# Kernel tuning notes

Hardware: AMD Instinct MI355X
Metric: run time of the kernel (lower is better)

Reference implementation:

```python
import jax, jax.numpy as jnp
import numpy as np

B, S, D, F, TOPK = 8, 2048, 1024, 64, 8


def setup_inputs() -> dict:
    key = jax.random.key(0)
    ks = jax.random.split(key, 4)
    scale = 1.0 / np.sqrt(D)
    return {
        "x": jax.random.normal(ks[0], (B, S, D), dtype=jnp.float32),
        "W_top": jax.random.normal(ks[1], (D, F), dtype=jnp.float32) * scale,
        "b_top": jnp.zeros((F,), dtype=jnp.float32),
        "W_feat": jax.random.normal(ks[2], (D, F), dtype=jnp.float32) * scale,
        "b_feat": jnp.zeros((F,), dtype=jnp.float32),
        "W_gates": jax.random.normal(ks[3], (F, D), dtype=jnp.float32) * scale,
        "b_gates": jnp.zeros((F,), dtype=jnp.float32),
        "alpha": jnp.ones((1,), dtype=jnp.float32),
        "num": TOPK,
    }


def reference(x, W_top, b_top, W_feat, b_feat, W_gates, b_gates, alpha, num):
    # Router logits and top-k selection: [B,S,F] -> vals/idx [B,S,num]
    top_logits = jnp.einsum("bsd,df->bsf", x, W_top) + b_top
    vals, idx = jax.lax.top_k(top_logits, num)
    sm = jax.nn.softmax(vals, axis=-1)                     # softmax over selected experts
    # Scatter softmax'd top-k weights into dense [B,S,F] (zeros elsewhere)
    onehot = jax.nn.one_hot(idx, F, dtype=sm.dtype)        # [B,S,num,F]
    type_dense = jnp.einsum("bsk,bskf->bsf", sm, onehot)
    # Dense softmax routing branch
    feat_soft = jax.nn.softmax(jnp.einsum("bsd,df->bsf", x, W_feat) + b_feat, axis=-1)
    a = jax.nn.sigmoid(alpha)                              # [1], broadcasts
    features = a * type_dense + (1.0 - a) * feat_soft      # [B,S,F]
    # num_feature small Linear(dims,1)+Sigmoid gates fused into one GEMM
    gates = jax.nn.sigmoid(jnp.einsum("bsd,fd->bsf", x, W_gates) + b_gates)  # [B,S,F]
    # Weighted sum over feature axis; original returns shape [B,S,1]
    return jnp.sum(gates * features, axis=-1, keepdims=True)
```

## Files before the change

kernel.cpp:

```cpp
#include <hip/hip_runtime.h>
#include <math.h>

#define D_DIM 1024
#define TOKB  32
#define NCH   32

typedef short  bf16x8 __attribute__((ext_vector_type(8)));
typedef float  f32x4  __attribute__((ext_vector_type(4)));

__device__ __forceinline__ ushort f2bf(float f) {
  uint u = __float_as_uint(f);
  return (ushort)((u + 0x7fffu + ((u >> 16) & 1u)) >> 16);
}
__device__ __forceinline__ float bf2f(ushort h) {
  return __uint_as_float(((uint)h) << 16);
}
__device__ __forceinline__ float sigm(float v) {
  return 1.f / (1.f + expf(-v));
}

__global__ __launch_bounds__(256) void pack_w_kernel(
    const float* __restrict__ Wt, const float* __restrict__ Wf,
    const float* __restrict__ Wg, ushort* __restrict__ Wp) {
  int gid = blockIdx.x * 256 + threadIdx.x;
  if (gid >= 32 * 12 * 64 * 4) return;
  int jp   = gid & 3;
  int t    = gid >> 2;
  int lane = t & 63;
  int t2   = t >> 6;
  int fb   = t2 % 12;
  int ks   = t2 / 12;
  int k0   = ks * 32 + ((lane >> 4) << 3) + jp * 2;
  int f    = fb * 16 + (lane & 15);
  float v0, v1;
  if (f < 64)       { v0 = Wt[k0 * 64 + f];            v1 = Wt[(k0 + 1) * 64 + f]; }
  else if (f < 128) { v0 = Wf[k0 * 64 + f - 64];       v1 = Wf[(k0 + 1) * 64 + f - 64]; }
  else              { v0 = Wg[(f - 128) * D_DIM + k0]; v1 = Wg[(f - 128) * D_DIM + k0 + 1]; }
  ushort h0 = f2bf(v0), h1 = f2bf(v1);
  ushort l0 = f2bf(v0 - bf2f(h0)), l1 = f2bf(v1 - bf2f(h1));
  size_t base = ((size_t)(ks * 12 + fb) * 2) * 512 + lane * 8 + jp * 2;
  *(uint*)(Wp + base)       = (uint)h0 | ((uint)h1 << 16);
  *(uint*)(Wp + base + 512) = (uint)l0 | ((uint)l1 << 16);
}

__global__ __launch_bounds__(256, 2) void moe_gate_kernel(
    const float* __restrict__ x, const ushort* __restrict__ Wp,
    const float* __restrict__ b_top, const float* __restrict__ b_feat,
    const float* __restrict__ b_gates, const float* __restrict__ alpha,
    const int* __restrict__ nump, float* __restrict__ out) {
  __shared__ float L[32 * 196 + 192];
  float* bsm = L + 32 * 196;
  const int tid  = threadIdx.x;
  const int lane = tid & 63;
  const int wid  = tid >> 6;
  const int wr   = wid >> 1;
  const int wc   = wid & 1;
  const int tok0 = blockIdx.x * TOKB;

  if (tid < 192)
    bsm[tid] = (tid < 64) ? b_top[tid]
             : (tid < 128) ? b_feat[tid - 64] : b_gates[tid - 128];

  const float* xrow = x + (size_t)(tok0 + wr * 16 + (lane & 15)) * D_DIM
                        + ((lane >> 4) << 3);
  const ushort* wbase = Wp + (size_t)(wc * 6) * 1024 + lane * 8;

  f32x4 acc[6] = {};
  f32x4 xa = *(const f32x4*)(xrow);
  f32x4 xb = *(const f32x4*)(xrow + 4);

  for (int c = 0; c < NCH; ++c) {
    bf16x8 ah, al;
#pragma unroll
    for (int i = 0; i < 8; ++i) {
      float v = (i < 4) ? xa[i] : xb[i - 4];
      ushort h = f2bf(v);
      ah[i] = (short)h;
      al[i] = (short)f2bf(v - bf2f(h));
    }
    int cn = (c < NCH - 1) ? c + 1 : c;
    xa = *(const f32x4*)(xrow + cn * 32);
    xb = *(const f32x4*)(xrow + cn * 32 + 4);

    const ushort* wp = wbase + (size_t)c * 12288;
#pragma unroll
    for (int fbl = 0; fbl < 6; ++fbl) {
      bf16x8 bh = *(const bf16x8*)(wp + fbl * 1024);
      bf16x8 bl = *(const bf16x8*)(wp + fbl * 1024 + 512);
      acc[fbl] = __builtin_amdgcn_mfma_f32_16x16x32_bf16(ah, bh, acc[fbl], 0, 0, 0);
      acc[fbl] = __builtin_amdgcn_mfma_f32_16x16x32_bf16(al, bh, acc[fbl], 0, 0, 0);
      acc[fbl] = __builtin_amdgcn_mfma_f32_16x16x32_bf16(ah, bl, acc[fbl], 0, 0, 0);
    }
    __builtin_amdgcn_s_barrier();
  }

  __syncthreads();
#pragma unroll
  for (int fbl = 0; fbl < 6; ++fbl) {
    int f = wc * 96 + fbl * 16 + (lane & 15);
    int t = wr * 16 + ((lane >> 4) << 2);
    float bv = bsm[f];
#pragma unroll
    for (int r = 0; r < 4; ++r)
      L[(t + r) * 196 + f] = acc[fbl][r] + bv;
  }
  __syncthreads();

  {
    const int t   = tid >> 3;
    const int sub = tid & 7;
    const float* Lr = L + t * 196;
    float tp[8], ftv[8], gtv[8];
#pragma unroll
    for (int j = 0; j < 8; ++j) {
      int f = sub + 8 * j;
      tp[j]  = Lr[f];
      ftv[j] = Lr[64 + f];
      gtv[j] = sigm(Lr[128 + f]);
    }
    float mf = ftv[0];
#pragma unroll
    for (int j = 1; j < 8; ++j) mf = fmaxf(mf, ftv[j]);
#pragma unroll
    for (int m = 1; m < 8; m <<= 1) mf = fmaxf(mf, __shfl_xor(mf, m, 8));
    float Zf = 0.f, Sf = 0.f;
#pragma unroll
    for (int j = 0; j < 8; ++j) {
      float e = expf(ftv[j] - mf);
      Zf += e;
      Sf = fmaf(gtv[j], e, Sf);
    }
#pragma unroll
    for (int m = 1; m < 8; m <<= 1) {
      Zf += __shfl_xor(Zf, m, 8);
      Sf += __shfl_xor(Sf, m, 8);
    }
    int num = *nump;
    num = num < 1 ? 1 : (num > 64 ? 64 : num);
    uint sel8 = 0;
    float m0 = 0.f, Zt = 0.f, St = 0.f;
    for (int k = 0; k < num; ++k) {
      float bv = -3.4e38f; int bj = -1;
#pragma unroll
      for (int j = 0; j < 8; ++j)
        if (!((sel8 >> j) & 1u) && tp[j] > bv) { bv = tp[j]; bj = j; }
      int bf = (bj >= 0) ? (sub + 8 * bj) : (1 << 30);
#pragma unroll
      for (int m = 1; m < 8; m <<= 1) {
        float ov = __shfl_xor(bv, m, 8);
        int   of = __shfl_xor(bf, m, 8);
        if (ov > bv || (ov == bv && of < bf)) { bv = ov; bf = of; }
      }
      if (k == 0) m0 = bv;
      float e = expf(bv - m0);
      Zt += e;
      St = fmaf(sigm(Lr[128 + bf]), e, St);
      if ((bf & 7) == sub) sel8 |= 1u << (bf >> 3);
    }
    if (sub == 0) {
      float a = sigm(alpha[0]);
      out[tok0 + t] = a * (St / Zt) + (1.f - a) * (Sf / Zf);
    }
  }
}

extern "C" void kernel_launch(void* const* d_in, const int* in_sizes, int n_in,
                              void* d_out, int out_size, void* d_ws, size_t ws_size,
                              hipStream_t stream) {
  const float* x       = (const float*)d_in[0];
  const float* W_top   = (const float*)d_in[1];
  const float* b_top   = (const float*)d_in[2];
  const float* W_feat  = (const float*)d_in[3];
  const float* b_feat  = (const float*)d_in[4];
  const float* W_gates = (const float*)d_in[5];
  const float* b_gates = (const float*)d_in[6];
  const float* alpha   = (const float*)d_in[7];
  const int*   nump    = (const int*)d_in[8];
  float*       out     = (float*)d_out;
  ushort*      Wp      = (ushort*)d_ws;

  int n_tok = in_sizes[0] / D_DIM;
  hipLaunchKernelGGL(pack_w_kernel, dim3(384), dim3(256), 0, stream,
                     W_top, W_feat, W_gates, Wp);
  hipLaunchKernelGGL(moe_gate_kernel, dim3(n_tok / TOKB), dim3(256), 0, stream,
                     x, Wp, b_top, b_feat, b_gates, alpha, nump, out);
}
```

Before: 155.4 us.

## Split K across warps with register double-buffered weight and x prefetch

Each block's four warps now split the 1024-long reduction into two halves instead of splitting tokens. Each warp covers all 32 tokens, so every weight fragment it loads feeds two token tiles. Weight and x fragments for the next chunk are loaded into a second register buffer while the current chunk computes, and the per-iteration barrier is gone. The two partial sums are combined in shared memory with an extra synchronisation step. This raises register pressure (24 accumulators plus 24 weight vectors), which may hurt occupancy under the two-blocks-per-CU launch bound.

```diff
diff --git a/kernel.cpp b/kernel.cpp
--- a/kernel.cpp
+++ b/kernel.cpp
@@ -3,7 +3,7 @@
 
 #define D_DIM 1024
 #define TOKB  32
-#define NCH   32
+#define KCH   16
 
 typedef short  bf16x8 __attribute__((ext_vector_type(8)));
 typedef float  f32x4  __attribute__((ext_vector_type(4)));
@@ -17,6 +17,16 @@
 }
 __device__ __forceinline__ float sigm(float v) {
   return 1.f / (1.f + expf(-v));
+}
+__device__ __forceinline__ void conv8(const f32x4 va, const f32x4 vb,
+                                      bf16x8& ah, bf16x8& al) {
+#pragma unroll
+  for (int i = 0; i < 8; ++i) {
+    float v = (i < 4) ? va[i] : vb[i - 4];
+    ushort h = f2bf(v);
+    ah[i] = (short)h;
+    al[i] = (short)f2bf(v - bf2f(h));
+  }
 }
 
 __global__ __launch_bounds__(256) void pack_w_kernel(
@@ -53,7 +63,7 @@
   const int tid  = threadIdx.x;
   const int lane = tid & 63;
   const int wid  = tid >> 6;
-  const int wr   = wid >> 1;
+  const int kh   = wid >> 1;
   const int wc   = wid & 1;
   const int tok0 = blockIdx.x * TOKB;
 
@@ -61,48 +71,82 @@
     bsm[tid] = (tid < 64) ? b_top[tid]
              : (tid < 128) ? b_feat[tid - 64] : b_gates[tid - 128];
 
-  const float* xrow = x + (size_t)(tok0 + wr * 16 + (lane & 15)) * D_DIM
-                        + ((lane >> 4) << 3);
-  const ushort* wbase = Wp + (size_t)(wc * 6) * 1024 + lane * 8;
-
-  f32x4 acc[6] = {};
-  f32x4 xa = *(const f32x4*)(xrow);
-  f32x4 xb = *(const f32x4*)(xrow + 4);
-
-  for (int c = 0; c < NCH; ++c) {
-    bf16x8 ah, al;
-#pragma unroll
-    for (int i = 0; i < 8; ++i) {
-      float v = (i < 4) ? xa[i] : xb[i - 4];
-      ushort h = f2bf(v);
-      ah[i] = (short)h;
-      al[i] = (short)f2bf(v - bf2f(h));
-    }
-    int cn = (c < NCH - 1) ? c + 1 : c;
-    xa = *(const f32x4*)(xrow + cn * 32);
-    xb = *(const f32x4*)(xrow + cn * 32 + 4);
-
-    const ushort* wp = wbase + (size_t)c * 12288;
-#pragma unroll
-    for (int fbl = 0; fbl < 6; ++fbl) {
-      bf16x8 bh = *(const bf16x8*)(wp + fbl * 1024);
-      bf16x8 bl = *(const bf16x8*)(wp + fbl * 1024 + 512);
-      acc[fbl] = __builtin_amdgcn_mfma_f32_16x16x32_bf16(ah, bh, acc[fbl], 0, 0, 0);
-      acc[fbl] = __builtin_amdgcn_mfma_f32_16x16x32_bf16(al, bh, acc[fbl], 0, 0, 0);
-      acc[fbl] = __builtin_amdgcn_mfma_f32_16x16x32_bf16(ah, bl, acc[fbl], 0, 0, 0);
-    }
-    __builtin_amdgcn_s_barrier();
-  }
+  const float* xp0 = x + (size_t)(tok0 + (lane & 15)) * D_DIM + kh * 512 + ((lane >> 4) << 3);
+  const float* xp1 = xp0 + (size_t)16 * D_DIM;
+  const ushort* wbase = Wp + (size_t)(kh * KCH) * 12288 + (size_t)(wc * 6) * 1024 + lane * 8;
+
+  f32x4 acc[2][6] = {};
+  bf16x8 bAh[6], bAl[6], bBh[6], bBl[6];
+  f32x4 xA[4], xB[4];
+
+#define LOADB(BH, BL, c) do {                                        \
+    const ushort* wp_ = wbase + (size_t)(c) * 12288;                 \
+    _Pragma("unroll")                                                \
+    for (int q = 0; q < 6; ++q) {                                    \
+      BH[q] = *(const bf16x8*)(wp_ + q * 1024);                      \
+      BL[q] = *(const bf16x8*)(wp_ + q * 1024 + 512);                \
+    } } while (0)
+#define LOADX(XR, c) do {                                            \
+    XR[0] = *(const f32x4*)(xp0 + (c) * 32);                         \
+    XR[1] = *(const f32x4*)(xp0 + (c) * 32 + 4);                     \
+    XR[2] = *(const f32x4*)(xp1 + (c) * 32);                         \
+    XR[3] = *(const f32x4*)(xp1 + (c) * 32 + 4); } while (0)
+#define COMPUTE(XR, BH, BL) do {                                     \
+    bf16x8 ah0, al0, ah1, al1;                                       \
+    conv8(XR[0], XR[1], ah0, al0);                                   \
+    conv8(XR[2], XR[3], ah1, al1);                                   \
+    _Pragma("unroll")                                                \
+    for (int q = 0; q < 6; ++q) {                                    \
+      acc[0][q] = __builtin_amdgcn_mfma_f32_16x16x32_bf16(ah0, BH[q], acc[0][q], 0, 0, 0); \
+      acc[0][q] = __builtin_amdgcn_mfma_f32_16x16x32_bf16(al0, BH[q], acc[0][q], 0, 0, 0); \
+      acc[0][q] = __builtin_amdgcn_mfma_f32_16x16x32_bf16(ah0, BL[q], acc[0][q], 0, 0, 0); \
+      acc[1][q] = __builtin_amdgcn_mfma_f32_16x16x32_bf16(ah1, BH[q], acc[1][q], 0, 0, 0); \
+      acc[1][q] = __builtin_amdgcn_mfma_f32_16x16x32_bf16(al1, BH[q], acc[1][q], 0, 0, 0); \
+      acc[1][q] = __builtin_amdgcn_mfma_f32_16x16x32_bf16(ah1, BL[q], acc[1][q], 0, 0, 0); \
+    } } while (0)
+
+  LOADB(bAh, bAl, 0);
+  LOADX(xA, 0);
+  for (int c = 0; c < KCH; c += 2) {
+    LOADB(bBh, bBl, c + 1);
+    LOADX(xB, c + 1);
+    COMPUTE(xA, bAh, bAl);
+    if (c + 2 < KCH) {
+      LOADB(bAh, bAl, c + 2);
+      LOADX(xA, c + 2);
+    }
+    COMPUTE(xB, bBh, bBl);
+  }
+#undef LOADB
+#undef LOADX
+#undef COMPUTE
 
   __syncthreads();
-#pragma unroll
-  for (int fbl = 0; fbl < 6; ++fbl) {
-    int f = wc * 96 + fbl * 16 + (lane & 15);
-    int t = wr * 16 + ((lane >> 4) << 2);
-    float bv = bsm[f];
-#pragma unroll
-    for (int r = 0; r < 4; ++r)
-      L[(t + r) * 196 + f] = acc[fbl][r] + bv;
+  if (kh == 0) {
+#pragma unroll
+    for (int tf = 0; tf < 2; ++tf)
+#pragma unroll
+      for (int q = 0; q < 6; ++q) {
+        int f = wc * 96 + q * 16 + (lane & 15);
+        int t = tf * 16 + ((lane >> 4) << 2);
+        float bv = bsm[f];
+#pragma unroll
+        for (int r = 0; r < 4; ++r)
+          L[(t + r) * 196 + f] = acc[tf][q][r] + bv;
+      }
+  }
+  __syncthreads();
+  if (kh == 1) {
+#pragma unroll
+    for (int tf = 0; tf < 2; ++tf)
+#pragma unroll
+      for (int q = 0; q < 6; ++q) {
+        int f = wc * 96 + q * 16 + (lane & 15);
+        int t = tf * 16 + ((lane >> 4) << 2);
+#pragma unroll
+        for (int r = 0; r < 4; ++r)
+          L[(t + r) * 196 + f] += acc[tf][q][r];
+      }
   }
   __syncthreads();
 
```

Result: faster. 141.0 us (-9.3%).
